# Optimization experiments

Hardware: AMD Instinct MI355X
Metric: run time of the kernel (lower is better)

Reference implementation:

```python
import jax, jax.numpy as jnp
import numpy as np

N, A, R = 131072, 16, 64


def setup_inputs() -> dict:
    key = jax.random.key(0)
    k1, k2, k3 = jax.random.split(key, 3)
    x = jax.random.normal(k1, (N, A), dtype=jnp.float32)
    mu = jax.random.uniform(k2, (R, A), dtype=jnp.float32)      # torch.rand(R, A)
    sigma = jnp.ones((R, A), dtype=jnp.float32) * 0.2           # torch.ones(R, A) * 0.2
    rho = jax.random.normal(k3, (R, A + 1), dtype=jnp.float32) * 0.1
    return {"x": x, "mu": mu, "sigma": sigma, "rho": rho}


def reference(x, mu, sigma, rho):
    # Rule consequents: z[k, r] = x[k] . rho[r, :A] + rho[r, A]   -> [N, R]
    z = jnp.einsum("na,ra->nr", x, rho[:, :-1]) + rho[:, -1]
    # Gaussian membership firing strengths (prod of exps == exp of sum):
    # w[k, r] = prod_a exp(-(x[k,a]-mu[r,a])^2 / (2 sigma[r,a]^2))
    d = x[:, None, :] - mu[None, :, :]                           # [N, R, A]
    logw = -jnp.sum(d * d / (2.0 * sigma[None] ** 2), axis=-1)   # [N, R]
    w = jnp.exp(logw)
    # diag(z @ w.T)[k] = sum_r z[k,r] * w[k,r]; normalized by rule-sum.
    num = jnp.sum(z * w, axis=1)
    den = jnp.sum(w, axis=1) + 1e-13
    return num / den
```

## Files before the change

### kernel.cpp

```cpp
#include <hip/hip_runtime.h>
#include <math.h>

#define NFEAT 16
#define NRULE 64
#define TPW 2

typedef _Float16 half8 __attribute__((ext_vector_type(8)));
typedef float    f4    __attribute__((ext_vector_type(4)));
union F4H8 { float4 f; half8 h; };

__global__ __launch_bounds__(256, 4) void fuzzy_fused(const float* __restrict__ x,
                                                      const float* __restrict__ mu,
                                                      const float* __restrict__ sigma,
                                                      const float* __restrict__ rho,
                                                      float* __restrict__ out, int n) {
    const float L2E = 1.4426950408889634f;
    const int tid  = threadIdx.x;
    const int L    = tid & 63;
    const int quad = L >> 4;
    const int m    = L & 15;
    const int wv   = __builtin_amdgcn_readfirstlane(tid >> 6);
    const int fb   = (quad & 1) * 8;

    const int tbase = (blockIdx.x * 4 + wv) * TPW;
    float4 xa[TPW], xb[TPW];
#pragma unroll
    for (int t = 0; t < TPW; ++t) {
        int tb = (tbase + t) * 16;
        int sc = tb + m < n ? tb + m : n - 1;
        const float4* xp = (const float4*)(x + (size_t)sc * NFEAT + fb);
        xa[t] = xp[0]; xb[t] = xp[1];
    }

    F4H8 b1[4], b2[4], r1[4], r2[4];
    float Pv[4], KLv[4], Bv[4];
    bool u = true;
#pragma unroll
    for (int T = 0; T < 4; ++T) {
        int rule = T * 16 + m;
        const float* mrow = mu    + rule * NFEAT + fb;
        const float* srow = sigma + rule * NFEAT + fb;
        const float* rrow = rho   + rule * (NFEAT + 1) + fb;
        float s0 = sigma[rule * NFEAT];
        float c0 = 1.0f / (2.0f * s0 * s0);
        float kp = 0.0f;
#pragma unroll
        for (int j = 0; j < 8; ++j) {
            float mm = mrow[j], ss = srow[j];
            float inv = 1.0f / (2.0f * ss * ss);
            u = u && (inv == c0);
            float Bw = 2.0f * inv * mm * L2E;
            _Float16 bh = (_Float16)Bw;
            b1[T].h[j] = bh;
            b2[T].h[j] = (_Float16)(Bw - (float)bh);
            float Rw = rrow[j];
            _Float16 rh_ = (_Float16)Rw;
            r1[T].h[j] = rh_;
            r2[T].h[j] = (_Float16)(Rw - (float)rh_);
            kp = fmaf(-inv * mm, mm, kp);
        }
        Pv[T]  = -c0 * L2E;
        KLv[T] = (kp + __shfl_xor(kp, 16)) * L2E;
        Bv[T]  = rho[rule * (NFEAT + 1) + NFEAT];
    }
    const int flag =
        __builtin_amdgcn_readfirstlane((int)(__ballot(u) == ~0ull));

    if (flag) {
#pragma unroll
        for (int t = 0; t < TPW; ++t) {
            int tb = (tbase + t) * 16;
            if (tb >= n) break;
            float xv[8] = {xa[t].x, xa[t].y, xa[t].z, xa[t].w,
                           xb[t].x, xb[t].y, xb[t].z, xb[t].w};
            F4H8 af;
            float qp = 0.0f;
#pragma unroll
            for (int j = 0; j < 8; ++j) {
                _Float16 h = (_Float16)xv[j];
                af.h[j] = (quad < 2) ? h : (_Float16)(xv[j] - (float)h);
                qp = fmaf(xv[j], xv[j], qp);
            }
            float Qf = qp + __shfl_xor(qp, 16);
            float Qr[4];
#pragma unroll
            for (int p = 0; p < 4; ++p) Qr[p] = __shfl(Qf, quad * 4 + p);

            f4 nsum = {0.f, 0.f, 0.f, 0.f}, dsum = {0.f, 0.f, 0.f, 0.f};
#pragma unroll
            for (int T = 0; T < 4; ++T) {
                f4 z4 = {0.f, 0.f, 0.f, 0.f};
                f4 accL = __builtin_amdgcn_mfma_f32_16x16x32_f16(af.h, b1[T].h, z4, 0, 0, 0);
                accL    = __builtin_amdgcn_mfma_f32_16x16x32_f16(af.h, b2[T].h, accL, 0, 0, 0);
                f4 accZ = __builtin_amdgcn_mfma_f32_16x16x32_f16(af.h, r1[T].h, z4, 0, 0, 0);
                accZ    = __builtin_amdgcn_mfma_f32_16x16x32_f16(af.h, r2[T].h, accZ, 0, 0, 0);
#pragma unroll
                for (int p = 0; p < 4; ++p) {
                    float l = fmaf(Pv[T], Qr[p], accL[p] + KLv[T]);
                    float w = __builtin_amdgcn_exp2f(l);
                    float zf = accZ[p] + Bv[T];
                    nsum[p] = fmaf(zf, w, nsum[p]);
                    dsum[p] += w;
                }
            }
#pragma unroll
            for (int d = 1; d < 16; d <<= 1) {
#pragma unroll
                for (int p = 0; p < 4; ++p) {
                    nsum[p] += __shfl_xor(nsum[p], d);
                    dsum[p] += __shfl_xor(dsum[p], d);
                }
            }
            if (m == 0) {
                float4 o;
                o.x = nsum[0] * __builtin_amdgcn_rcpf(dsum[0] + 1e-13f);
                o.y = nsum[1] * __builtin_amdgcn_rcpf(dsum[1] + 1e-13f);
                o.z = nsum[2] * __builtin_amdgcn_rcpf(dsum[2] + 1e-13f);
                o.w = nsum[3] * __builtin_amdgcn_rcpf(dsum[3] + 1e-13f);
                ((float4*)(out + tb))[quad] = o;
            }
        }
    } else {
#pragma unroll
        for (int t = 0; t < TPW; ++t) {
            int tb = (tbase + t) * 16;
            if (tb >= n) break;
            int s = tb + m;
            const float4* xp = (const float4*)(x + (size_t)s * NFEAT);
            float4 a = xp[0], b = xp[1], c = xp[2], d = xp[3];
            float xs[NFEAT] = {a.x,a.y,a.z,a.w, b.x,b.y,b.z,b.w,
                               c.x,c.y,c.z,c.w, d.x,d.y,d.z,d.w};
            float num = 0.0f, den = 0.0f;
            for (int r = quad * 16; r < quad * 16 + 16; ++r) {
                float z = rho[r * (NFEAT + 1) + NFEAT];
                float l = 0.0f;
                for (int aa = 0; aa < NFEAT; ++aa) {
                    float mm = mu[r * NFEAT + aa];
                    float ss = sigma[r * NFEAT + aa];
                    float inv = 1.0f / (2.0f * ss * ss);
                    float dd = xs[aa] - mm;
                    l = fmaf(-inv * dd, dd, l);
                    z = fmaf(rho[r * (NFEAT + 1) + aa], xs[aa], z);
                }
                float w = __builtin_amdgcn_exp2f(l * L2E);
                num = fmaf(z, w, num);
                den += w;
            }
            num += __shfl_xor(num, 16); den += __shfl_xor(den, 16);
            num += __shfl_xor(num, 32); den += __shfl_xor(den, 32);
            if (L < 16) out[tb + L] = num / (den + 1e-13f);
        }
    }
}

extern "C" void kernel_launch(void* const* d_in, const int* in_sizes, int n_in,
                              void* d_out, int out_size, void* d_ws, size_t ws_size,
                              hipStream_t stream) {
    const float* x     = (const float*)d_in[0];
    const float* mu    = (const float*)d_in[1];
    const float* sigma = (const float*)d_in[2];
    const float* rho   = (const float*)d_in[3];
    float* out = (float*)d_out;

    int n = in_sizes[0] / NFEAT;

    int blocks = (n + 16 * 4 * TPW - 1) / (16 * 4 * TPW);
    fuzzy_fused<<<blocks, 256, 0, stream>>>(x, mu, sigma, rho, out, n);
}
```

Baseline: 79.17 us.

## Handle per-feature sigma via extra MFMA on x^2, drop uniform-sigma fast path

Expands the Gaussian exponent as a matrix product of [x^2, x] against split-fp16 weights [-1/(2σ²), 2μ/(2σ²)], so per-feature sigma is handled on the MFMA path. This removes the uniform-sigma ballot check and the scalar fallback branch, along with the Qf shuffles. It adds two MFMAs per rule tile, more weight registers, and relaxes launch bounds to 3 waves per SIMD. It also swaps an exact divide for rcpf.

```diff
diff --git a/kernel.cpp b/kernel.cpp
--- a/kernel.cpp
+++ b/kernel.cpp
@@ -9,7 +9,7 @@
 typedef float    f4    __attribute__((ext_vector_type(4)));
 union F4H8 { float4 f; half8 h; };
 
-__global__ __launch_bounds__(256, 4) void fuzzy_fused(const float* __restrict__ x,
+__global__ __launch_bounds__(256, 3) void fuzzy_fused(const float* __restrict__ x,
                                                       const float* __restrict__ mu,
                                                       const float* __restrict__ sigma,
                                                       const float* __restrict__ rho,
@@ -32,123 +32,87 @@
         xa[t] = xp[0]; xb[t] = xp[1];
     }
 
-    F4H8 b1[4], b2[4], r1[4], r2[4];
-    float Pv[4], KLv[4], Bv[4];
-    bool u = true;
+    F4H8 c1[4], c2[4], b1[4], b2[4], r1[4], r2[4];
+    float Kv[4], Bv[4];
 #pragma unroll
     for (int T = 0; T < 4; ++T) {
         int rule = T * 16 + m;
         const float* mrow = mu    + rule * NFEAT + fb;
         const float* srow = sigma + rule * NFEAT + fb;
         const float* rrow = rho   + rule * (NFEAT + 1) + fb;
-        float s0 = sigma[rule * NFEAT];
-        float c0 = 1.0f / (2.0f * s0 * s0);
         float kp = 0.0f;
 #pragma unroll
         for (int j = 0; j < 8; ++j) {
-            float mm = mrow[j], ss = srow[j];
-            float inv = 1.0f / (2.0f * ss * ss);
-            u = u && (inv == c0);
-            float Bw = 2.0f * inv * mm * L2E;
+            float mm = mrow[j], ss = srow[j], rr = rrow[j];
+            float iv = __builtin_amdgcn_rcpf(2.0f * ss * ss);
+            float Cw = -iv * L2E;
+            _Float16 ch = (_Float16)Cw;
+            c1[T].h[j] = ch;
+            c2[T].h[j] = (_Float16)(Cw - (float)ch);
+            float Bw = 2.0f * iv * mm * L2E;
             _Float16 bh = (_Float16)Bw;
             b1[T].h[j] = bh;
             b2[T].h[j] = (_Float16)(Bw - (float)bh);
-            float Rw = rrow[j];
-            _Float16 rh_ = (_Float16)Rw;
+            _Float16 rh_ = (_Float16)rr;
             r1[T].h[j] = rh_;
-            r2[T].h[j] = (_Float16)(Rw - (float)rh_);
-            kp = fmaf(-inv * mm, mm, kp);
+            r2[T].h[j] = (_Float16)(rr - (float)rh_);
+            kp = fmaf(iv * mm, mm, kp);
         }
-        Pv[T]  = -c0 * L2E;
-        KLv[T] = (kp + __shfl_xor(kp, 16)) * L2E;
-        Bv[T]  = rho[rule * (NFEAT + 1) + NFEAT];
+        Kv[T] = -(kp + __shfl_xor(kp, 16)) * L2E;
+        Bv[T] = rho[rule * (NFEAT + 1) + NFEAT];
     }
-    const int flag =
-        __builtin_amdgcn_readfirstlane((int)(__ballot(u) == ~0ull));
 
-    if (flag) {
 #pragma unroll
-        for (int t = 0; t < TPW; ++t) {
-            int tb = (tbase + t) * 16;
-            if (tb >= n) break;
-            float xv[8] = {xa[t].x, xa[t].y, xa[t].z, xa[t].w,
-                           xb[t].x, xb[t].y, xb[t].z, xb[t].w};
-            F4H8 af;
-            float qp = 0.0f;
+    for (int t = 0; t < TPW; ++t) {
+        int tb = (tbase + t) * 16;
+        if (tb >= n) break;
+        float xv[8] = {xa[t].x, xa[t].y, xa[t].z, xa[t].w,
+                       xb[t].x, xb[t].y, xb[t].z, xb[t].w};
+        F4H8 a1, a2;
 #pragma unroll
-            for (int j = 0; j < 8; ++j) {
-                _Float16 h = (_Float16)xv[j];
-                af.h[j] = (quad < 2) ? h : (_Float16)(xv[j] - (float)h);
-                qp = fmaf(xv[j], xv[j], qp);
-            }
-            float Qf = qp + __shfl_xor(qp, 16);
-            float Qr[4];
+        for (int j = 0; j < 8; ++j) {
+            float v = xv[j];
+            _Float16 h = (_Float16)v;
+            a1.h[j] = (quad < 2) ? h : (_Float16)(v - (float)h);
+            float s = v * v;
+            _Float16 hs = (_Float16)s;
+            a2.h[j] = (quad < 2) ? hs : (_Float16)(s - (float)hs);
+        }
+
+        f4 nsum = {0.f, 0.f, 0.f, 0.f}, dsum = {0.f, 0.f, 0.f, 0.f};
 #pragma unroll
-            for (int p = 0; p < 4; ++p) Qr[p] = __shfl(Qf, quad * 4 + p);
-
-            f4 nsum = {0.f, 0.f, 0.f, 0.f}, dsum = {0.f, 0.f, 0.f, 0.f};
+        for (int T = 0; T < 4; ++T) {
+            f4 z4 = {0.f, 0.f, 0.f, 0.f};
+            f4 accG = __builtin_amdgcn_mfma_f32_16x16x32_f16(a2.h, c1[T].h, z4, 0, 0, 0);
+            accG    = __builtin_amdgcn_mfma_f32_16x16x32_f16(a2.h, c2[T].h, accG, 0, 0, 0);
+            accG    = __builtin_amdgcn_mfma_f32_16x16x32_f16(a1.h, b1[T].h, accG, 0, 0, 0);
+            accG    = __builtin_amdgcn_mfma_f32_16x16x32_f16(a1.h, b2[T].h, accG, 0, 0, 0);
+            f4 accZ = __builtin_amdgcn_mfma_f32_16x16x32_f16(a1.h, r1[T].h, z4, 0, 0, 0);
+            accZ    = __builtin_amdgcn_mfma_f32_16x16x32_f16(a1.h, r2[T].h, accZ, 0, 0, 0);
 #pragma unroll
-            for (int T = 0; T < 4; ++T) {
-                f4 z4 = {0.f, 0.f, 0.f, 0.f};
-                f4 accL = __builtin_amdgcn_mfma_f32_16x16x32_f16(af.h, b1[T].h, z4, 0, 0, 0);
-                accL    = __builtin_amdgcn_mfma_f32_16x16x32_f16(af.h, b2[T].h, accL, 0, 0, 0);
-                f4 accZ = __builtin_amdgcn_mfma_f32_16x16x32_f16(af.h, r1[T].h, z4, 0, 0, 0);
-                accZ    = __builtin_amdgcn_mfma_f32_16x16x32_f16(af.h, r2[T].h, accZ, 0, 0, 0);
-#pragma unroll
-                for (int p = 0; p < 4; ++p) {
-                    float l = fmaf(Pv[T], Qr[p], accL[p] + KLv[T]);
-                    float w = __builtin_amdgcn_exp2f(l);
-                    float zf = accZ[p] + Bv[T];
-                    nsum[p] = fmaf(zf, w, nsum[p]);
-                    dsum[p] += w;
-                }
-            }
-#pragma unroll
-            for (int d = 1; d < 16; d <<= 1) {
-#pragma unroll
-                for (int p = 0; p < 4; ++p) {
-                    nsum[p] += __shfl_xor(nsum[p], d);
-                    dsum[p] += __shfl_xor(dsum[p], d);
-                }
-            }
-            if (m == 0) {
-                float4 o;
-                o.x = nsum[0] * __builtin_amdgcn_rcpf(dsum[0] + 1e-13f);
-                o.y = nsum[1] * __builtin_amdgcn_rcpf(dsum[1] + 1e-13f);
-                o.z = nsum[2] * __builtin_amdgcn_rcpf(dsum[2] + 1e-13f);
-                o.w = nsum[3] * __builtin_amdgcn_rcpf(dsum[3] + 1e-13f);
-                ((float4*)(out + tb))[quad] = o;
+            for (int p = 0; p < 4; ++p) {
+                float l = accG[p] + Kv[T];
+                float w = __builtin_amdgcn_exp2f(l);
+                float zf = accZ[p] + Bv[T];
+                nsum[p] = fmaf(zf, w, nsum[p]);
+                dsum[p] += w;
             }
         }
-    } else {
 #pragma unroll
-        for (int t = 0; t < TPW; ++t) {
-            int tb = (tbase + t) * 16;
-            if (tb >= n) break;
-            int s = tb + m;
-            const float4* xp = (const float4*)(x + (size_t)s * NFEAT);
-            float4 a = xp[0], b = xp[1], c = xp[2], d = xp[3];
-            float xs[NFEAT] = {a.x,a.y,a.z,a.w, b.x,b.y,b.z,b.w,
-                               c.x,c.y,c.z,c.w, d.x,d.y,d.z,d.w};
-            float num = 0.0f, den = 0.0f;
-            for (int r = quad * 16; r < quad * 16 + 16; ++r) {
-                float z = rho[r * (NFEAT + 1) + NFEAT];
-                float l = 0.0f;
-                for (int aa = 0; aa < NFEAT; ++aa) {
-                    float mm = mu[r * NFEAT + aa];
-                    float ss = sigma[r * NFEAT + aa];
-                    float inv = 1.0f / (2.0f * ss * ss);
-                    float dd = xs[aa] - mm;
-                    l = fmaf(-inv * dd, dd, l);
-                    z = fmaf(rho[r * (NFEAT + 1) + aa], xs[aa], z);
-                }
-                float w = __builtin_amdgcn_exp2f(l * L2E);
-                num = fmaf(z, w, num);
-                den += w;
+        for (int d = 1; d < 16; d <<= 1) {
+#pragma unroll
+            for (int p = 0; p < 4; ++p) {
+                nsum[p] += __shfl_xor(nsum[p], d);
+                dsum[p] += __shfl_xor(dsum[p], d);
             }
-            num += __shfl_xor(num, 16); den += __shfl_xor(den, 16);
-            num += __shfl_xor(num, 32); den += __shfl_xor(den, 32);
-            if (L < 16) out[tb + L] = num / (den + 1e-13f);
+        }
+        if (m == 0) {
+            float4 o;
+            o.x = nsum[0] * __builtin_amdgcn_rcpf(dsum[0] + 1e-13f);
+            o.y = nsum[1] * __builtin_amdgcn_rcpf(dsum[1] + 1e-13f);
+            o.z = nsum[2] * __builtin_amdgcn_rcpf(dsum[2] + 1e-13f);
+            o.w = nsum[3] * __builtin_amdgcn_rcpf(dsum[3] + 1e-13f);
+            ((float4*)(out + tb))[quad] = o;
         }
     }
 }
```

Measured after the change: 77.32 us. 1.02x faster.
